# Performance work log

Hardware: AMD Instinct MI355X
Metric: run time of the kernel (lower is better)

## Reference

```python
import jax, jax.numpy as jnp
import numpy as np

N_NODES = 100000
N_FEAT = 512
HIDDEN = 16
N_CLASSES = 40
N_EDGES = 3200000


def gcn_conv(x, edge_index, W, b, n_nodes):
    # PyG GCNConv: linear transform, then symmetric-normalized aggregation
    # over A + I (self-loops added), aggregating source -> target.
    h = x @ W  # [N, out]
    loops = jnp.arange(n_nodes, dtype=edge_index.dtype)
    src = jnp.concatenate([edge_index[0], loops])
    dst = jnp.concatenate([edge_index[1], loops])
    ones = jnp.ones(src.shape[0], dtype=h.dtype)
    deg = jax.ops.segment_sum(ones, dst, num_segments=n_nodes)  # in-degree incl. self-loop
    dinv = jnp.where(deg > 0, jax.lax.rsqrt(deg), 0.0)
    norm = dinv[src] * dinv[dst]  # [E+N]
    msg = h[src] * norm[:, None]
    out = jax.ops.segment_sum(msg, dst, num_segments=n_nodes)
    return out + b


def setup_inputs() -> dict:
    key = jax.random.key(0)
    k1, k2, k3, k4 = jax.random.split(key, 4)
    x = jax.random.normal(k1, (N_NODES, N_FEAT), dtype=jnp.float32)
    edge_index = jax.random.randint(k2, (2, N_EDGES), 0, N_NODES, dtype=jnp.int32)
    # Glorot-style init for the two GCNConv layers
    W1 = jax.random.normal(k3, (N_FEAT, HIDDEN), dtype=jnp.float32) / np.sqrt(N_FEAT)
    b1 = jnp.zeros((HIDDEN,), dtype=jnp.float32)
    W2 = jax.random.normal(k4, (HIDDEN, N_CLASSES), dtype=jnp.float32) / np.sqrt(HIDDEN)
    b2 = jnp.zeros((N_CLASSES,), dtype=jnp.float32)
    return {"x": x, "edge_index": edge_index, "W1": W1, "b1": b1, "W2": W2, "b2": b2}


def reference(x, edge_index, W1, b1, W2, b2):
    n = x.shape[0]
    h = gcn_conv(x, edge_index, W1, b1, n)
    h = jax.nn.relu(h)
    # F.dropout with training=False (eval mode) is the identity
    h = gcn_conv(h, edge_index, W2, b2, n)
    return jax.nn.log_softmax(h, axis=1)
```

## Files before the change

### kernel.cpp

```cpp
#include <hip/hip_runtime.h>
#include <math.h>

#define FEAT 512
#define HID  16
#define NCLS 40

#define CAPB  18432
#define CHUNK 4096
#define RPT   16
#define BPAD  16

__global__ __launch_bounds__(256) void bin2_kernel(const int* __restrict__ src,
                                                   const int* __restrict__ dst,
                                                   int* __restrict__ bcnt,
                                                   unsigned* __restrict__ bpack, int E) {
    __shared__ unsigned lsort[CHUNK];
    __shared__ int hist[256];
    __shared__ int lstart[257];
    __shared__ int gbase[256];
    __shared__ int ss[256];

    int t = threadIdx.x;
    int e0 = blockIdx.x * CHUNK;

    hist[t] = 0;
    __syncthreads();

    unsigned rec[RPT];
    int bkt[RPT];
#pragma unroll
    for (int i = 0; i < RPT; ++i) {
        int ee = e0 + i * 256 + t;
        bkt[i] = -1;
        if (ee < E) {
            int d = dst[ee];
            int s = src[ee];
            bkt[i] = d >> 9;
            rec[i] = (unsigned)s | ((unsigned)(d & 511) << 17);
            atomicAdd(&hist[bkt[i]], 1);
        }
    }
    __syncthreads();

    int v = hist[t];
    ss[t] = v;
    __syncthreads();
    for (int o = 1; o < 256; o <<= 1) {
        int add = (t >= o) ? ss[t - o] : 0;
        __syncthreads();
        ss[t] += add;
        __syncthreads();
    }
    lstart[t] = ss[t] - v;
    if (t == 255) lstart[256] = ss[255];
    if (v > 0) gbase[t] = atomicAdd(&bcnt[t * BPAD], v);
    hist[t] = 0;
    __syncthreads();

#pragma unroll
    for (int i = 0; i < RPT; ++i) {
        if (bkt[i] >= 0) {
            int p = atomicAdd(&hist[bkt[i]], 1);
            lsort[lstart[bkt[i]] + p] = rec[i];
        }
    }
    __syncthreads();

    int nrec = lstart[256];
    for (int j = t; j < nrec; j += 256) {
        int lo = 0, hi = 255;
        while (lo < hi) {
            int mid = (lo + hi + 1) >> 1;
            if (lstart[mid] <= j) lo = mid; else hi = mid - 1;
        }
        bpack[(size_t)lo * CAPB + gbase[lo] + (j - lstart[lo])] = lsort[j];
    }
}

__global__ void bscan_kernel(const int* __restrict__ bcnt, int* __restrict__ boff, int nbuck) {
    __shared__ int s[256];
    int t = threadIdx.x;
    int v = (t < nbuck) ? bcnt[t * BPAD] : 0;
    s[t] = v;
    __syncthreads();
    for (int o = 1; o < 256; o <<= 1) {
        int add = (t >= o) ? s[t - o] : 0;
        __syncthreads();
        s[t] += add;
        __syncthreads();
    }
    if (t <= nbuck) boff[t] = (t > 0) ? s[t - 1] : 0;
}

__global__ __launch_bounds__(256) void bucket_build_kernel(const unsigned* __restrict__ bpack,
                                                           const int* __restrict__ boff,
                                                           int* __restrict__ off,
                                                           float* __restrict__ dinv,
                                                           int* __restrict__ csr,
                                                           int N, int E) {
    __shared__ int cnt[512];
    __shared__ int ptr[512];
    __shared__ int ss[256];
    int b = blockIdx.x;
    int t = threadIdx.x;
    int base = b << 9;
    int nn = min(512, N - base);

    cnt[t] = 0;
    cnt[t + 256] = 0;
    __syncthreads();

    int r0 = boff[b], r1 = boff[b + 1];
    int nrec = r1 - r0;
    const unsigned* bp = bpack + (size_t)b * CAPB;

    for (int j = t; j < nrec; j += 256) {
        unsigned rec = bp[j];
        atomicAdd(&cnt[rec >> 17], 1);
    }
    __syncthreads();

    int a0 = cnt[2 * t], a1 = cnt[2 * t + 1];
    int tsum = a0 + a1;
    ss[t] = tsum;
    __syncthreads();
    for (int o = 1; o < 256; o <<= 1) {
        int add = (t >= o) ? ss[t - o] : 0;
        __syncthreads();
        ss[t] += add;
        __syncthreads();
    }
    int excl = (t > 0) ? ss[t - 1] : 0;

    int p0 = r0 + excl;
    int p1 = p0 + a0;
    ptr[2 * t] = p0;
    ptr[2 * t + 1] = p1;
    if (2 * t < nn) {
        off[base + 2 * t] = p0;
        dinv[base + 2 * t] = rsqrtf((float)a0 + 1.0f);
    }
    if (2 * t + 1 < nn) {
        off[base + 2 * t + 1] = p1;
        dinv[base + 2 * t + 1] = rsqrtf((float)a1 + 1.0f);
    }
    __syncthreads();

    for (int j = t; j < nrec; j += 256) {
        unsigned rec = bp[j];
        int p = atomicAdd(&ptr[rec >> 17], 1);
        csr[p] = rec & 131071u;
    }

    if (b == (int)gridDim.x - 1 && t == 0) off[N] = E;
}

__global__ __launch_bounds__(256) void gemm1_kernel(const float* __restrict__ x,
                                                    const float* __restrict__ W1,
                                                    float* __restrict__ h1, int N) {
    __shared__ float4 xt4[16 * 129];
    __shared__ float4 wt4[16 * 129];
    int t = threadIdx.x;

    float* wt = (float*)wt4;
#pragma unroll
    for (int i = 0; i < 32; ++i) {
        int f = t + i * 256;
        int k = f >> 4, o = f & 15;
        wt[o * 516 + k] = W1[f];
    }

    int base = blockIdx.x * 16;
    {
        const float4* xg = (const float4*)(x + (size_t)base * FEAT);
#pragma unroll
        for (int i = 0; i < 8; ++i) {
            int f = t + i * 256;
            int r = f >> 7, k4 = f & 127;
            xt4[r * 129 + k4] = xg[r * 128 + k4];
        }
    }
    __syncthreads();

    int r = t >> 4, o = t & 15;
    const float4* xr = (const float4*)((const float*)xt4 + r * 516);
    const float4* wr = (const float4*)((const float*)wt4 + o * 516);
    float acc = 0.f;
#pragma unroll 8
    for (int k = 0; k < 128; ++k) {
        float4 a = xr[k];
        float4 b = wr[k];
        acc += a.x * b.x + a.y * b.y + a.z * b.z + a.w * b.w;
    }
    h1[(size_t)(base + r) * HID + o] = acc;
}

template <bool RELU>
__global__ __launch_bounds__(256) void agg_kernel(const float* __restrict__ h,
                                                  const float* __restrict__ dinv,
                                                  const int* __restrict__ off,
                                                  const int* __restrict__ csr,
                                                  const float* __restrict__ bias,
                                                  float* __restrict__ out, int N) {
    int wave = (blockIdx.x * 256 + threadIdx.x) >> 6;
    int lane = threadIdx.x & 63;
    if (wave >= N) return;
    int i = wave;
    int nb = lane >> 4, f = lane & 15;
    int o0 = off[i];
    int ne = off[i + 1] - o0;
    float acc = 0.f;
    for (int b = 0; b < ne; b += 4) {
        int j = b + nb;
        if (j < ne) {
            int s = csr[o0 + j];
            acc += dinv[s] * h[s * HID + f];
        }
    }
    acc += __shfl_xor(acc, 16);
    acc += __shfl_xor(acc, 32);
    float di = dinv[i];
    float v = di * (acc + di * h[i * HID + f]);
    if (bias) v += bias[f];
    if (RELU) v = fmaxf(v, 0.f);
    if (lane < 16) out[i * HID + f] = v;
}

__global__ __launch_bounds__(256) void final_kernel(const float* __restrict__ g,
                                                    const float* __restrict__ W2,
                                                    const float* __restrict__ b2,
                                                    float* __restrict__ out, int N) {
    __shared__ float w2s[HID * NCLS];
    __shared__ float b2s[NCLS];
    int t = threadIdx.x;
    for (int f = t; f < HID * NCLS; f += 256) w2s[f] = W2[f];
    if (t < NCLS) b2s[t] = b2[t];
    __syncthreads();

    int wave = (blockIdx.x * 256 + t) >> 6;
    int lane = t & 63;
    if (wave >= N) return;
    int i = wave;

    float acc = 0.f;
    float v = -1e30f;
    if (lane < NCLS) {
        acc = b2s[lane];
        const float* gr = g + (size_t)i * HID;
#pragma unroll
        for (int k = 0; k < HID; ++k) acc += gr[k] * w2s[k * NCLS + lane];
        v = acc;
    }
    for (int d = 32; d >= 1; d >>= 1) v = fmaxf(v, __shfl_xor(v, d));
    float e = (lane < NCLS) ? __expf(acc - v) : 0.f;
    float s = e;
    for (int d = 32; d >= 1; d >>= 1) s += __shfl_xor(s, d);
    if (lane < NCLS) out[(size_t)i * NCLS + lane] = acc - v - __logf(s);
}


extern "C" void kernel_launch(void* const* d_in, const int* in_sizes, int n_in,
                              void* d_out, int out_size, void* d_ws, size_t ws_size,
                              hipStream_t stream) {
    const float* x  = (const float*)d_in[0];
    const int*   ei = (const int*)d_in[1];
    const float* W1 = (const float*)d_in[2];
    const float* b1 = (const float*)d_in[3];
    const float* W2 = (const float*)d_in[4];
    const float* b2 = (const float*)d_in[5];

    int N = in_sizes[0] / FEAT;
    int E = in_sizes[1] / 2;
    const int* src = ei;
    const int* dst = ei + E;

    char* ws = (char*)d_ws;
    size_t p = 0;
    auto alloc = [&](size_t bytes) -> void* {
        void* r = ws + p;
        p = (p + bytes + 15) & ~(size_t)15;
        return r;
    };
    int*   off  = (int*)alloc((size_t)(N + 1) * 4);
    float* dinv = (float*)alloc((size_t)N * 4);
    int*   csr  = (int*)alloc((size_t)E * 4);
    float* h1   = (float*)alloc((size_t)N * HID * 4);
    float* a1   = (float*)alloc((size_t)N * HID * 4);
    float* g    = (float*)alloc((size_t)N * HID * 4);
    int*   bcnt = (int*)alloc((size_t)256 * BPAD * 4);
    int*   boff = (int*)alloc((size_t)257 * 4);

    unsigned* bpack = (unsigned*)h1;

    int nbuck = (N + 511) >> 9;
    int nbin  = (E + CHUNK - 1) / CHUNK;

    hipMemsetAsync(bcnt, 0, (size_t)256 * BPAD * 4, stream);
    bin2_kernel<<<nbin, 256, 0, stream>>>(src, dst, bcnt, bpack, E);
    bscan_kernel<<<1, 256, 0, stream>>>(bcnt, boff, nbuck);
    bucket_build_kernel<<<nbuck, 256, 0, stream>>>(bpack, boff, off, dinv, csr, N, E);

    gemm1_kernel<<<N / 16, 256, 0, stream>>>(x, W1, h1, N);
    agg_kernel<true><<<(N + 3) / 4, 256, 0, stream>>>(h1, dinv, off, csr, b1, a1, N);
    agg_kernel<false><<<(N + 3) / 4, 256, 0, stream>>>(a1, dinv, off, csr, nullptr, g, N);
    final_kernel<<<(N + 3) / 4, 256, 0, stream>>>(g, W2, b2, (float*)d_out, N);
}
```

Baseline: 618.1 us.

## Vectorize neighbor aggregation with float4 lanes and fuse second aggregation with classifier

```diff
diff --git a/kernel.cpp b/kernel.cpp
--- a/kernel.cpp
+++ b/kernel.cpp
@@ -195,41 +195,56 @@
     h1[(size_t)(base + r) * HID + o] = acc;
 }
 
-template <bool RELU>
-__global__ __launch_bounds__(256) void agg_kernel(const float* __restrict__ h,
-                                                  const float* __restrict__ dinv,
-                                                  const int* __restrict__ off,
-                                                  const int* __restrict__ csr,
-                                                  const float* __restrict__ bias,
-                                                  float* __restrict__ out, int N) {
+__global__ __launch_bounds__(256) void agg1_kernel(const float* __restrict__ h,
+                                                   const float* __restrict__ dinv,
+                                                   const int* __restrict__ off,
+                                                   const int* __restrict__ csr,
+                                                   const float* __restrict__ bias,
+                                                   float* __restrict__ out, int N) {
     int wave = (blockIdx.x * 256 + threadIdx.x) >> 6;
     int lane = threadIdx.x & 63;
     if (wave >= N) return;
     int i = wave;
-    int nb = lane >> 4, f = lane & 15;
+    int nb = lane >> 2, q = lane & 3;
     int o0 = off[i];
     int ne = off[i + 1] - o0;
-    float acc = 0.f;
-    for (int b = 0; b < ne; b += 4) {
+    float4 acc = {0.f, 0.f, 0.f, 0.f};
+    for (int b = 0; b < ne; b += 16) {
         int j = b + nb;
         if (j < ne) {
             int s = csr[o0 + j];
-            acc += dinv[s] * h[s * HID + f];
-        }
-    }
-    acc += __shfl_xor(acc, 16);
-    acc += __shfl_xor(acc, 32);
-    float di = dinv[i];
-    float v = di * (acc + di * h[i * HID + f]);
-    if (bias) v += bias[f];
-    if (RELU) v = fmaxf(v, 0.f);
-    if (lane < 16) out[i * HID + f] = v;
-}
-
-__global__ __launch_bounds__(256) void final_kernel(const float* __restrict__ g,
-                                                    const float* __restrict__ W2,
-                                                    const float* __restrict__ b2,
-                                                    float* __restrict__ out, int N) {
+            float w = dinv[s];
+            float4 hv = *(const float4*)(h + (size_t)s * HID + q * 4);
+            acc.x += w * hv.x; acc.y += w * hv.y;
+            acc.z += w * hv.z; acc.w += w * hv.w;
+        }
+    }
+    for (int d = 4; d <= 32; d <<= 1) {
+        acc.x += __shfl_xor(acc.x, d);
+        acc.y += __shfl_xor(acc.y, d);
+        acc.z += __shfl_xor(acc.z, d);
+        acc.w += __shfl_xor(acc.w, d);
+    }
+    if (lane < 4) {
+        float di = dinv[i];
+        float4 hs = *(const float4*)(h + (size_t)i * HID + q * 4);
+        float4 b4 = *(const float4*)(bias + q * 4);
+        float4 v;
+        v.x = fmaxf(di * (acc.x + di * hs.x) + b4.x, 0.f);
+        v.y = fmaxf(di * (acc.y + di * hs.y) + b4.y, 0.f);
+        v.z = fmaxf(di * (acc.z + di * hs.z) + b4.z, 0.f);
+        v.w = fmaxf(di * (acc.w + di * hs.w) + b4.w, 0.f);
+        *(float4*)(out + (size_t)i * HID + q * 4) = v;
+    }
+}
+
+__global__ __launch_bounds__(256) void agg2_final_kernel(const float* __restrict__ h,
+                                                         const float* __restrict__ dinv,
+                                                         const int* __restrict__ off,
+                                                         const int* __restrict__ csr,
+                                                         const float* __restrict__ W2,
+                                                         const float* __restrict__ b2,
+                                                         float* __restrict__ out, int N) {
     __shared__ float w2s[HID * NCLS];
     __shared__ float b2s[NCLS];
     int t = threadIdx.x;
@@ -241,21 +256,51 @@
     int lane = t & 63;
     if (wave >= N) return;
     int i = wave;
-
-    float acc = 0.f;
-    float v = -1e30f;
-    if (lane < NCLS) {
-        acc = b2s[lane];
-        const float* gr = g + (size_t)i * HID;
-#pragma unroll
-        for (int k = 0; k < HID; ++k) acc += gr[k] * w2s[k * NCLS + lane];
-        v = acc;
-    }
+    int nb = lane >> 2, q = lane & 3;
+    int o0 = off[i];
+    int ne = off[i + 1] - o0;
+    float4 acc = {0.f, 0.f, 0.f, 0.f};
+    for (int b = 0; b < ne; b += 16) {
+        int j = b + nb;
+        if (j < ne) {
+            int s = csr[o0 + j];
+            float w = dinv[s];
+            float4 hv = *(const float4*)(h + (size_t)s * HID + q * 4);
+            acc.x += w * hv.x; acc.y += w * hv.y;
+            acc.z += w * hv.z; acc.w += w * hv.w;
+        }
+    }
+    for (int d = 4; d <= 32; d <<= 1) {
+        acc.x += __shfl_xor(acc.x, d);
+        acc.y += __shfl_xor(acc.y, d);
+        acc.z += __shfl_xor(acc.z, d);
+        acc.w += __shfl_xor(acc.w, d);
+    }
+    float di = dinv[i];
+    float4 hs = *(const float4*)(h + (size_t)i * HID + q * 4);
+    float4 g4;
+    g4.x = di * (acc.x + di * hs.x);
+    g4.y = di * (acc.y + di * hs.y);
+    g4.z = di * (acc.z + di * hs.z);
+    g4.w = di * (acc.w + di * hs.w);
+
+    bool act = lane < NCLS;
+    int lw = act ? lane : 0;
+    float accv = 0.f;
+#pragma unroll
+    for (int k = 0; k < HID; ++k) {
+        float comp = ((k & 3) == 0) ? g4.x : ((k & 3) == 1) ? g4.y
+                   : ((k & 3) == 2) ? g4.z : g4.w;
+        float gb = __shfl(comp, k >> 2);
+        accv += gb * w2s[k * NCLS + lw];
+    }
+    accv += b2s[lw];
+    float v = act ? accv : -1e30f;
     for (int d = 32; d >= 1; d >>= 1) v = fmaxf(v, __shfl_xor(v, d));
-    float e = (lane < NCLS) ? __expf(acc - v) : 0.f;
+    float e = act ? __expf(accv - v) : 0.f;
     float s = e;
     for (int d = 32; d >= 1; d >>= 1) s += __shfl_xor(s, d);
-    if (lane < NCLS) out[(size_t)i * NCLS + lane] = acc - v - __logf(s);
+    if (act) out[(size_t)i * NCLS + lane] = accv - v - __logf(s);
 }
 
 
@@ -286,9 +331,10 @@
     int*   csr  = (int*)alloc((size_t)E * 4);
     float* h1   = (float*)alloc((size_t)N * HID * 4);
     float* a1   = (float*)alloc((size_t)N * HID * 4);
-    float* g    = (float*)alloc((size_t)N * HID * 4);
+    float* pad  = (float*)alloc((size_t)N * HID * 4);
     int*   bcnt = (int*)alloc((size_t)256 * BPAD * 4);
     int*   boff = (int*)alloc((size_t)257 * 4);
+    (void)pad;
 
     unsigned* bpack = (unsigned*)h1;
 
@@ -301,7 +347,7 @@
     bucket_build_kernel<<<nbuck, 256, 0, stream>>>(bpack, boff, off, dinv, csr, N, E);
 
     gemm1_kernel<<<N / 16, 256, 0, stream>>>(x, W1, h1, N);
-    agg_kernel<true><<<(N + 3) / 4, 256, 0, stream>>>(h1, dinv, off, csr, b1, a1, N);
-    agg_kernel<false><<<(N + 3) / 4, 256, 0, stream>>>(a1, dinv, off, csr, nullptr, g, N);
-    final_kernel<<<(N + 3) / 4, 256, 0, stream>>>(g, W2, b2, (float*)d_out, N);
-}
+    agg1_kernel<<<(N + 3) / 4, 256, 0, stream>>>(h1, dinv, off, csr, b1, a1, N);
+    agg2_final_kernel<<<(N + 3) / 4, 256, 0, stream>>>(a1, dinv, off, csr, W2, b2,
+                                                       (float*)d_out, N);
+}
```

Result: faster. 531.2 us (-14.1%).
